# Optimization experiments

Hardware: AMD Instinct MI355X
Metric: run time of the kernel (lower is better)

The kernel has to match this reference:

```python
import jax, jax.numpy as jnp
import numpy as np

H = 128      # hidden_channels
G = 512      # number of graphs in the batch
NEG_SLOPE = 0.2


def _seg_sum(x, idx, n):
    return jax.ops.segment_sum(x, idx, num_segments=n)


def _sage(x_src, x_dst, ei, Wl, bl, Wr):
    # PyG SAGEConv: lin_l(mean_j x_j) + lin_r(x_i); lin_l has bias, lin_r does not.
    s, d = ei[0], ei[1]
    n = x_dst.shape[0]
    agg = _seg_sum(x_src[s], d, n)
    cnt = _seg_sum(jnp.ones((ei.shape[1],), x_src.dtype), d, n)
    mean = agg / jnp.maximum(cnt, 1.0)[:, None]
    return mean @ Wl + bl + x_dst @ Wr


def _gat(x_src, x_dst, ei, Ws, Wd, a_s, a_d, b):
    # PyG GATConv (heads=1, add_self_loops=False, bipartite): segment softmax over dst.
    s, d = ei[0], ei[1]
    n = x_dst.shape[0]
    hs = x_src @ Ws                                  # [N_src, H]
    hd = x_dst @ Wd                                  # [N_dst, H]
    logit = jax.nn.leaky_relu((hs @ a_s)[s] + (hd @ a_d)[d], NEG_SLOPE)
    m = jax.ops.segment_max(logit, d, num_segments=n)
    e = jnp.exp(logit - m[d])
    z = _seg_sum(e, d, n)
    alpha = e / jnp.maximum(z[d], 1e-16)
    return _seg_sum(alpha[:, None] * hs[s], d, n) + b


def _gcn(x, ei, W, b):
    # PyG GCNConv with add_self_loops=True, normalize=True (same src/dst node type).
    s, d = ei[0], ei[1]
    n = x.shape[0]
    deg = _seg_sum(jnp.ones((ei.shape[1],), x.dtype), d, n) + 1.0  # +1 self loop
    dis = jax.lax.rsqrt(deg)
    h = x @ W
    norm = dis[s] * dis[d]
    out = _seg_sum(norm[:, None] * h[s], d, n) + (dis * dis)[:, None] * h
    return out + b


def _pool(x, b):
    s = _seg_sum(x, b, G)
    c = _seg_sum(jnp.ones((x.shape[0],), x.dtype), b, G)
    return s / jnp.maximum(c, 1.0)[:, None]


def setup_inputs() -> dict:
    key = jax.random.key(0)
    ks = iter(jax.random.split(key, 80))
    scale = 1.0 / np.sqrt(H)

    def nrm(shape, sc=scale):
        return jax.random.normal(next(ks), shape, jnp.float32) * sc

    def edges(e, n_src, n_dst):
        src = jax.random.randint(next(ks), (e,), 0, n_src, jnp.int32)
        dst = jax.random.randint(next(ks), (e,), 0, n_dst, jnp.int32)
        return jnp.stack([src, dst])

    def batch(n):
        return jnp.sort(jax.random.randint(next(ks), (n,), 0, G, jnp.int32))

    N_CD, N_SEQ, N_ANNO, N_RANGE, N_MD = 100000, 80000, 80000, 80000, 50000
    inp = {
        'x_cd': nrm((N_CD, H), 1.0), 'x_seq': nrm((N_SEQ, H), 1.0),
        'x_anno': nrm((N_ANNO, H), 1.0), 'x_range': nrm((N_RANGE, H), 1.0),
        'x_md': nrm((N_MD, H), 1.0),
        'ei_seq': edges(160000, N_CD, N_SEQ),
        'ei_anno': edges(200000, N_CD, N_ANNO),
        'ei_range': edges(200000, N_CD, N_RANGE),
        'ei_comp': edges(300000, N_MD, N_CD),
        'ei_cc': edges(300000, N_CD, N_CD),
        'ei_mm': edges(150000, N_MD, N_MD),
        'b_cd': batch(N_CD), 'b_seq': batch(N_SEQ), 'b_anno': batch(N_ANNO),
        'b_range': batch(N_RANGE), 'b_md': batch(N_MD),
    }
    # per-layer stacked params (leading axis = 2 layers)
    for nm, shp in [('Wsl_seq', (2, H, H)), ('bs_seq', (2, H)), ('Wsr_seq', (2, H, H)),
                    ('Wsl_anno', (2, H, H)), ('bs_anno', (2, H)), ('Wsr_anno', (2, H, H)),
                    ('Wg_comp_s', (2, H, H)), ('Wg_comp_d', (2, H, H)),
                    ('ag_comp_s', (2, H)), ('ag_comp_d', (2, H)), ('bg_comp', (2, H)),
                    ('Wg_range_s', (2, H, H)), ('Wg_range_d', (2, H, H)),
                    ('ag_range_s', (2, H)), ('ag_range_d', (2, H)), ('bg_range', (2, H)),
                    ('Wc_cc', (2, H, H)), ('bc_cc', (2, H)),
                    ('Wc_mm', (2, H, H)), ('bc_mm', (2, H)),
                    ('lin1_W', (5 * H, H)), ('lin1_b', (H,)),
                    ('lin2_W', (H, 1)), ('lin2_b', (1,))]:
        inp[nm] = nrm(shp)
    return inp


def reference(x_cd, x_seq, x_anno, x_range, x_md,
              ei_seq, ei_anno, ei_range, ei_comp, ei_cc, ei_mm,
              b_cd, b_seq, b_anno, b_range, b_md,
              Wsl_seq, bs_seq, Wsr_seq, Wsl_anno, bs_anno, Wsr_anno,
              Wg_comp_s, Wg_comp_d, ag_comp_s, ag_comp_d, bg_comp,
              Wg_range_s, Wg_range_d, ag_range_s, ag_range_d, bg_range,
              Wc_cc, bc_cc, Wc_mm, bc_mm,
              lin1_W, lin1_b, lin2_W, lin2_b):
    for l in range(2):
        # HeteroConv aggr='sum': CD receives GAT(MD->CD) + GCN(CD->CD)
        n_cd = (_gat(x_md, x_cd, ei_comp, Wg_comp_s[l], Wg_comp_d[l],
                     ag_comp_s[l], ag_comp_d[l], bg_comp[l])
                + _gcn(x_cd, ei_cc, Wc_cc[l], bc_cc[l]))
        n_seq = _sage(x_cd, x_seq, ei_seq, Wsl_seq[l], bs_seq[l], Wsr_seq[l])
        n_anno = _sage(x_cd, x_anno, ei_anno, Wsl_anno[l], bs_anno[l], Wsr_anno[l])
        n_range = _gat(x_cd, x_range, ei_range, Wg_range_s[l], Wg_range_d[l],
                       ag_range_s[l], ag_range_d[l], bg_range[l])
        n_md = _gcn(x_md, ei_mm, Wc_mm[l], bc_mm[l])
        x_cd, x_seq, x_anno, x_range, x_md = (
            jax.nn.relu(n_cd), jax.nn.relu(n_seq), jax.nn.relu(n_anno),
            jax.nn.relu(n_range), jax.nn.relu(n_md))
    emb = jnp.concatenate([_pool(x_cd, b_cd), _pool(x_seq, b_seq),
                           _pool(x_anno, b_anno), _pool(x_range, b_range),
                           _pool(x_md, b_md)], axis=-1)        # [G, 5H]
    h = jax.nn.relu(emb @ lin1_W + lin1_b)  # Dropout(0.7) is identity in eval
    return (h @ lin2_W + lin2_b).reshape(-1)  # [G]
```

## Files before the change

kernel.cpp:

```cpp
#include <hip/hip_runtime.h>

#define HD 128
#define GNUM 512
#define RPB 520
#define IDXCAP 512
#define TM 32

typedef __attribute__((ext_vector_type(8))) short short8v;
typedef __attribute__((ext_vector_type(4))) float f32x4;

__device__ __forceinline__ void split1(float a, short& h, short& l) {
  unsigned u = __float_as_uint(a);
  unsigned hb = (u + 0x7FFFu + ((u >> 16) & 1u)) & 0xFFFF0000u;
  h = (short)(hb >> 16);
  float rest = a - __uint_as_float(hb);
  unsigned u2 = __float_as_uint(rest);
  l = (short)((u2 + 0x7FFFu + ((u2 >> 16) & 1u)) >> 16);
}

struct WTab { const float* p[8]; };
__global__ __launch_bounds__(256) void k_split_w(WTab tab, short* __restrict__ whi,
                                                 short* __restrict__ wlo)
{
  int m = blockIdx.x >> 6;
  int i = (blockIdx.x & 63) * 256 + threadIdx.x;
  const float* W = tab.p[m >> 1] + (m & 1) * 16384;
  int k = i >> 7, n = i & 127;
  short h, l;
  split1(W[k * 128 + n], h, l);
  whi[m * 16384 + n * 128 + k] = h;
  wlo[m * 16384 + n * 128 + k] = l;
}

#define CF_LD 132
__global__ __launch_bounds__(256) void k_gemm_conv(
    const float* __restrict__ A1, const short* __restrict__ WH1, const short* __restrict__ WL1,
    const int* __restrict__ grp, const int* __restrict__ gcol, int mode,
    const float* __restrict__ wsrc, const float* __restrict__ rowsc,
    const float* __restrict__ A2, const short* __restrict__ WH2, const short* __restrict__ WL2,
    float* __restrict__ C, const float* __restrict__ bias, const float* addin,
    int N, int relu,
    const float* __restrict__ avec, float* __restrict__ adot,
    const float* __restrict__ avec2, float* __restrict__ adot2)
{
  __shared__ char smem[TM * 136 * 2 * 2];
  __shared__ int idxbuf[IDXCAP];
  __shared__ float wbuf[IDXCAP];
  short* Ah = (short*)smem;
  short* Al = Ah + TM * 136;
  float* Cf = (float*)smem;

  const int t = threadIdx.x;
  const int row0 = blockIdx.x * TM;
  const int lane = t & 63, wid = t >> 6;
  const int g = lane >> 4, cn = lane & 15;
  const int colbase = wid * 32;

  f32x4 zero = {0.f, 0.f, 0.f, 0.f};
  f32x4 acc[2][2];
#pragma unroll
  for (int rt = 0; rt < 2; ++rt) { acc[rt][0] = zero; acc[rt][1] = zero; }

  auto storeAhl = [&](int row, int ln, float4 s) {
    short4 h, l;
    split1(s.x, h.x, l.x); split1(s.y, h.y, l.y);
    split1(s.z, h.z, l.z); split1(s.w, h.w, l.w);
    *(short4*)(Ah + row * 136 + ln * 4) = h;
    *(short4*)(Al + row * 136 + ln * 4) = l;
  };

  auto stageA = [&](const float* __restrict__ A) {
    const float4* A4 = (const float4*)(A + (size_t)row0 * 128);
#pragma unroll
    for (int i = 0; i < 4; ++i) {
      int f4 = t + i * 256;
      int row = f4 >> 5, c4 = f4 & 31;
      float4 v = make_float4(0.f, 0.f, 0.f, 0.f);
      if (row0 + row < N) v = A4[f4];
      storeAhl(row, c4, v);
    }
  };

  auto getcw = [&](int e, int e_lo, int& c, float& w) {
    int off = e - e_lo;
    if (off < IDXCAP) { c = idxbuf[off]; w = wbuf[off]; }
    else { c = gcol[e]; w = wsrc ? wsrc[c] : 0.f; }
  };

  auto stage_gather = [&](const float* __restrict__ X, int e_lo) {
#pragma unroll
    for (int i = 0; i < 4; ++i) {
      int f4 = t + i * 256;
      int row = f4 >> 5, ln = f4 & 31;
      int r = row0 + row;
      float4 s = make_float4(0.f, 0.f, 0.f, 0.f);
      int e0 = 0, e1 = 0;
      float rs = 0.f;
      if (r < N) {
        e0 = grp[r]; e1 = grp[r + 1];
        if (mode >= 2) rs = rowsc[r];
      }
      float z = 0.f;
      if (mode == 2 && r < N) {
        float4 xs_ = *(const float4*)(X + (size_t)r * 128 + ln * 4);
        float rr = rs * rs;
        s.x = rr * xs_.x; s.y = rr * xs_.y; s.z = rr * xs_.z; s.w = rr * xs_.w;
      }
      int e = e0;
      for (; e + 1 < e1; e += 2) {
        int c0, c1; float w0, w1;
        getcw(e, e_lo, c0, w0);
        getcw(e + 1, e_lo, c1, w1);
        float p0, p1;
        if (mode == 3) {
          float v0 = w0 + rs; v0 = v0 > 0.f ? v0 : 0.2f * v0;
          float v1 = w1 + rs; v1 = v1 > 0.f ? v1 : 0.2f * v1;
          p0 = __expf(v0); p1 = __expf(v1); z += p0 + p1;
        } else if (mode == 2) { p0 = w0 * rs; p1 = w1 * rs; }
        else { p0 = 1.f; p1 = 1.f; }
        float4 a = *(const float4*)(X + (size_t)c0 * 128 + ln * 4);
        float4 b = *(const float4*)(X + (size_t)c1 * 128 + ln * 4);
        s.x += p0 * a.x + p1 * b.x; s.y += p0 * a.y + p1 * b.y;
        s.z += p0 * a.z + p1 * b.z; s.w += p0 * a.w + p1 * b.w;
      }
      if (e < e1) {
        int c; float w;
        getcw(e, e_lo, c, w);
        float p;
        if (mode == 3) {
          float v = w + rs; v = v > 0.f ? v : 0.2f * v;
          p = __expf(v); z += p;
        } else if (mode == 2) p = w * rs;
        else p = 1.f;
        float4 a = *(const float4*)(X + (size_t)c * 128 + ln * 4);
        s.x += p * a.x; s.y += p * a.y; s.z += p * a.z; s.w += p * a.w;
      }
      if (mode == 1) {
        float inv = 1.f / fmaxf((float)(e1 - e0), 1.f);
        s.x *= inv; s.y *= inv; s.z *= inv; s.w *= inv;
      } else if (mode == 3) {
        float inv = (e1 > e0) ? 1.f / z : 0.f;
        s.x *= inv; s.y *= inv; s.z *= inv; s.w *= inv;
      }
      storeAhl(row, ln, s);
    }
  };

  auto accum = [&](const short* __restrict__ WH, const short* __restrict__ WL) {
#pragma unroll
    for (int kg = 0; kg < 4; ++kg) {
      short8v bhi[2], blo[2];
#pragma unroll
      for (int ct = 0; ct < 2; ++ct) {
        size_t o = (size_t)(colbase + ct * 16 + cn) * 128 + kg * 32 + g * 8;
        bhi[ct] = *(const short8v*)(WH + o);
        blo[ct] = *(const short8v*)(WL + o);
      }
#pragma unroll
      for (int rt = 0; rt < 2; ++rt) {
        const int ao = (rt * 16 + cn) * 136 + kg * 32 + g * 8;
        const short8v ah = *(const short8v*)(Ah + ao);
        const short8v al = *(const short8v*)(Al + ao);
#pragma unroll
        for (int ct = 0; ct < 2; ++ct) {
          acc[rt][ct] = __builtin_amdgcn_mfma_f32_16x16x32_bf16(ah, bhi[ct], acc[rt][ct], 0, 0, 0);
          acc[rt][ct] = __builtin_amdgcn_mfma_f32_16x16x32_bf16(al, bhi[ct], acc[rt][ct], 0, 0, 0);
          acc[rt][ct] = __builtin_amdgcn_mfma_f32_16x16x32_bf16(ah, blo[ct], acc[rt][ct], 0, 0, 0);
        }
      }
    }
  };

  if (mode != 0) {
    const int row_end = min(row0 + TM, N);
    const int e_lo = grp[row0];
    const int cnt = min(grp[row_end] - e_lo, IDXCAP);
    for (int k = t; k < cnt; k += 256) {
      int idx = gcol[e_lo + k];
      idxbuf[k] = idx;
      if (wsrc) wbuf[k] = wsrc[idx];
    }
    __syncthreads();
    stage_gather(A1, e_lo);
  } else {
    stageA(A1);
  }
  __syncthreads();
  accum(WH1, WL1);
  if (A2) {
    __syncthreads();
    stageA(A2);
    __syncthreads();
    accum(WH2, WL2);
  }
  __syncthreads();

#pragma unroll
  for (int rt = 0; rt < 2; ++rt)
#pragma unroll
    for (int ct = 0; ct < 2; ++ct)
#pragma unroll
      for (int r = 0; r < 4; ++r)
        Cf[(rt * 16 + g * 4 + r) * CF_LD + colbase + ct * 16 + cn] = acc[rt][ct][r];
  __syncthreads();

  float4* C4 = (float4*)(C + (size_t)row0 * 128);
#pragma unroll
  for (int i = 0; i < 4; ++i) {
    int f4 = t + i * 256;
    int row = f4 >> 5, c4 = f4 & 31;
    if (row0 + row < N) {
      float4 v = *(const float4*)(Cf + row * CF_LD + c4 * 4);
      if (bias) {
        float4 bv = *(const float4*)(bias + c4 * 4);
        v.x += bv.x; v.y += bv.y; v.z += bv.z; v.w += bv.w;
      }
      if (addin) {
        float4 av = *(const float4*)(addin + (size_t)(row0 + row) * 128 + c4 * 4);
        v.x += av.x; v.y += av.y; v.z += av.z; v.w += av.w;
      }
      if (relu) {
        v.x = fmaxf(v.x, 0.f); v.y = fmaxf(v.y, 0.f);
        v.z = fmaxf(v.z, 0.f); v.w = fmaxf(v.w, 0.f);
      }
      C4[f4] = v;
      if (avec) {
        float4 av = *(const float4*)(avec + c4 * 4);
        float p = v.x * av.x + v.y * av.y + v.z * av.z + v.w * av.w;
#pragma unroll
        for (int o = 1; o < 32; o <<= 1) p += __shfl_xor(p, o);
        if (c4 == 0) adot[row0 + row] = p;
      }
      if (avec2) {
        float4 av = *(const float4*)(avec2 + c4 * 4);
        float p = v.x * av.x + v.y * av.y + v.z * av.z + v.w * av.w;
#pragma unroll
        for (int o = 1; o < 32; o <<= 1) p += __shfl_xor(p, o);
        if (c4 == 0) adot2[row0 + row] = p;
      }
    }
  }
}

__global__ void k_rowdot(const float* __restrict__ x, const float* __restrict__ a,
                         float* __restrict__ out, int N)
{
  int wid = blockIdx.x * 4 + (threadIdx.x >> 6);
  int lane = threadIdx.x & 63;
  if (wid >= N) return;
  float2 xv = ((const float2*)x)[(size_t)wid * 64 + lane];
  float2 av = ((const float2*)a)[lane];
  float v = fmaf(xv.y, av.y, xv.x * av.x);
#pragma unroll
  for (int o = 32; o > 0; o >>= 1) v += __shfl_down(v, o);
  if (lane == 0) out[wid] = v;
}

__global__ void k_rowdot2(const float* __restrict__ x, const float* __restrict__ a1,
                          const float* __restrict__ a2, float* __restrict__ o1,
                          float* __restrict__ o2, int N)
{
  int wid = blockIdx.x * 4 + (threadIdx.x >> 6);
  int lane = threadIdx.x & 63;
  if (wid >= N) return;
  float2 xv = ((const float2*)x)[(size_t)wid * 64 + lane];
  float2 av1 = ((const float2*)a1)[lane];
  float2 av2 = ((const float2*)a2)[lane];
  float v1 = fmaf(xv.y, av1.y, xv.x * av1.x);
  float v2 = fmaf(xv.y, av2.y, xv.x * av2.x);
#pragma unroll
  for (int o = 32; o > 0; o >>= 1) { v1 += __shfl_down(v1, o); v2 += __shfl_down(v2, o); }
  if (lane == 0) { o1[wid] = v1; o2[wid] = v2; }
}

struct MTab { const float* W[8]; const float* a[8]; };
__global__ __launch_bounds__(128) void k_matvec8(MTab tb, float* __restrict__ wv)
{
  __shared__ float as[128];
  int m = blockIdx.x, i = threadIdx.x;
  as[i] = tb.a[m][i];
  __syncthreads();
  const float* W = tb.W[m];
  float v = 0.f;
  for (int j = 0; j < 128; ++j) v = fmaf(W[i * 128 + j], as[j], v);
  wv[m * 128 + i] = v;
}

struct HTab { const int* key[6]; int* cnt[6]; unsigned short* rank[6]; int bo[7]; int n[6]; };
__global__ void k_hist_rank_all(HTab tb) {
  int bi = blockIdx.x, ty = 0;
  while (ty < 5 && bi >= tb.bo[ty + 1]) ++ty;
  int i = (bi - tb.bo[ty]) * 256 + threadIdx.x;
  if (i < tb.n[ty])
    tb.rank[ty][i] = (unsigned short)atomicAdd(&tb.cnt[ty][tb.key[ty][i]], 1);
}

struct FTab { const int* es[6]; const int* ed[6]; const int* rp[6];
              const unsigned short* rank[6]; int* col[6]; int bo[7]; int n[6]; };
__global__ void k_fill_all(FTab tb) {
  int bi = blockIdx.x, ty = 0;
  while (ty < 5 && bi >= tb.bo[ty + 1]) ++ty;
  int e = (bi - tb.bo[ty]) * 256 + threadIdx.x;
  if (e >= tb.n[ty]) return;
  int p = tb.rp[ty][tb.ed[ty][e]] + (int)tb.rank[ty][e];
  tb.col[ty][p] = tb.es[ty][e];
}

struct STab { int* rp[6]; int* bs[6]; int n[6]; int bo[7]; };

__global__ __launch_bounds__(256) void k_scan_partial_all(STab tb) {
  __shared__ int red[256];
  int bi = blockIdx.x, ty = 0;
  while (ty < 5 && bi >= tb.bo[ty + 1]) ++ty;
  int lb = bi - tb.bo[ty];
  const int* rp = tb.rp[ty];
  const int N = tb.n[ty];
  const int t = threadIdx.x, base = lb * 4096;
  int s = 0;
  for (int i = t; i < 4096; i += 256) {
    int idx = base + i;
    if (idx < N) s += rp[idx];
  }
  red[t] = s;
  __syncthreads();
  for (int ofs = 128; ofs > 0; ofs >>= 1) {
    if (t < ofs) red[t] += red[t + ofs];
    __syncthreads();
  }
  if (t == 0) tb.bs[ty][lb] = red[0];
}

__global__ __launch_bounds__(256) void k_scan_bsums_all(STab tb) {
  __shared__ int sh[256];
  const int ty = blockIdx.x;
  const int nb = (tb.n[ty] + 4095) / 4096;
  const int t = threadIdx.x;
  int v = (t < nb) ? tb.bs[ty][t] : 0;
  sh[t] = v;
  __syncthreads();
  for (int ofs = 1; ofs < 256; ofs <<= 1) {
    int u = (t >= ofs) ? sh[t - ofs] : 0;
    __syncthreads();
    sh[t] += u;
    __syncthreads();
  }
  if (t < nb) tb.bs[ty][t] = sh[t] - v;
  if (t == 255) tb.rp[ty][tb.n[ty]] = sh[255];
}

__global__ __launch_bounds__(256) void k_scan_final_all(STab tb) {
  __shared__ int sh[4096 + 256];
  __shared__ int tsum[256];
  int bi = blockIdx.x, ty = 0;
  while (ty < 5 && bi >= tb.bo[ty + 1]) ++ty;
  int lb = bi - tb.bo[ty];
  int* rp = tb.rp[ty];
  const int N = tb.n[ty];
  const int t = threadIdx.x, base = lb * 4096;
  auto mp = [](int i) { return i + (i >> 4); };
#pragma unroll
  for (int i = 0; i < 16; ++i) {
    int idx = base + i * 256 + t;
    sh[mp(i * 256 + t)] = (idx < N) ? rp[idx] : 0;
  }
  __syncthreads();
  int s = 0;
#pragma unroll
  for (int j = 0; j < 16; ++j) s += sh[mp(t * 16 + j)];
  tsum[t] = s;
  __syncthreads();
  for (int ofs = 1; ofs < 256; ofs <<= 1) {
    int u = (t >= ofs) ? tsum[t - ofs] : 0;
    __syncthreads();
    tsum[t] += u;
    __syncthreads();
  }
  int pre = tsum[t] - s + tb.bs[ty][lb];
#pragma unroll
  for (int j = 0; j < 16; ++j) {
    int v = sh[mp(t * 16 + j)];
    sh[mp(t * 16 + j)] = pre;
    pre += v;
  }
  __syncthreads();
#pragma unroll
  for (int i = 0; i < 16; ++i) {
    int idx = base + i * 256 + t;
    if (idx < N) rp[idx] = sh[mp(i * 256 + t)];
  }
}

struct BTab { const int* b[5]; int n[5]; };
__global__ __launch_bounds__(512) void k_runptr(BTab tb, int* __restrict__ rpb_all) {
  const int ty = blockIdx.x;
  const int* b = tb.b[ty];
  const int N = tb.n[ty];
  const int t = threadIdx.x;
  int lo = 0, hi = N;
  while (lo < hi) {
    int mid = (lo + hi) >> 1;
    if (b[mid] < t) lo = mid + 1; else hi = mid;
  }
  rpb_all[ty * RPB + t] = lo;
  if (t == 0) rpb_all[ty * RPB + GNUM] = N;
}

struct DTab { const int* rp[2]; float* dis[2]; int n[2]; int bo[3]; };
__global__ void k_dis2(DTab tb) {
  int bi = blockIdx.x, ty = (bi >= tb.bo[1]) ? 1 : 0;
  int n = (bi - tb.bo[ty]) * 256 + threadIdx.x;
  if (n < tb.n[ty]) tb.dis[ty][n] = rsqrtf((float)(tb.rp[ty][n + 1] - tb.rp[ty][n]) + 1.f);
}

__global__ __launch_bounds__(256) void k_pool_seg(
    const float* __restrict__ x, const int* __restrict__ rpb,
    float* __restrict__ pool, int col_off)
{
  __shared__ float2 red2[4][64];
  const int g = blockIdx.x;
  const int t = threadIdx.x, w = t >> 6, lane = t & 63;
  const int n0 = rpb[g], n1 = rpb[g + 1];
  const float2* x2 = (const float2*)x;
  float a0 = 0.f, a1 = 0.f, b0 = 0.f, b1 = 0.f;
  int n = n0 + w;
  for (; n + 4 < n1; n += 8) {
    float2 vA = x2[(size_t)n * 64 + lane];
    float2 vB = x2[(size_t)(n + 4) * 64 + lane];
    a0 += vA.x; a1 += vA.y; b0 += vB.x; b1 += vB.y;
  }
  if (n < n1) { float2 vA = x2[(size_t)n * 64 + lane]; a0 += vA.x; a1 += vA.y; }
  red2[w][lane] = make_float2(a0 + b0, a1 + b1);
  __syncthreads();
  if (t < 64) {
    float2 r0 = red2[0][t], r1 = red2[1][t], r2 = red2[2][t], r3 = red2[3][t];
    float inv = 1.f / fmaxf((float)(n1 - n0), 1.f);
    ((float2*)(pool + (size_t)g * 640 + col_off))[t] =
        make_float2((r0.x + r1.x + r2.x + r3.x) * inv,
                    (r0.y + r1.y + r2.y + r3.y) * inv);
  }
}

__global__ void k_mlp(const float* __restrict__ pool,
                      const float* __restrict__ W1, const float* __restrict__ b1,
                      const float* __restrict__ W2, const float* __restrict__ b2,
                      float* __restrict__ out)
{
  __shared__ float emb[640];
  __shared__ float red[128];
  const int g = blockIdx.x, t = threadIdx.x;
  for (int i = t; i < 640; i += 128) emb[i] = pool[(size_t)g * 640 + i];
  __syncthreads();
  float acc = b1[t];
  for (int i = 0; i < 640; ++i) acc = fmaf(emb[i], W1[i * 128 + t], acc);
  float h = fmaxf(acc, 0.f);
  red[t] = h * W2[t];
  __syncthreads();
  for (int s = 64; s > 0; s >>= 1) {
    if (t < s) red[t] += red[t + s];
    __syncthreads();
  }
  if (t == 0) out[g] = red[0] + b2[0];
}

extern "C" void kernel_launch(void* const* d_in, const int* in_sizes, int n_in,
                              void* d_out, int out_size, void* d_ws, size_t ws_size,
                              hipStream_t stream)
{
  auto fin = [&](int i) { return (const float*)d_in[i]; };
  auto iin = [&](int i) { return (const int*)d_in[i]; };

  const float *x_cd = fin(0), *x_seq = fin(1), *x_anno = fin(2), *x_range = fin(3), *x_md = fin(4);
  const int *ei_seq = iin(5), *ei_anno = iin(6), *ei_range = iin(7),
            *ei_comp = iin(8), *ei_cc = iin(9), *ei_mm = iin(10);
  const int *b_cd = iin(11), *b_seq = iin(12), *b_anno = iin(13), *b_range = iin(14), *b_md = iin(15);

  const int N_CD = in_sizes[0] / HD, N_SEQ = in_sizes[1] / HD, N_ANNO = in_sizes[2] / HD,
            N_RANGE = in_sizes[3] / HD, N_MD = in_sizes[4] / HD;
  const int E_seq = in_sizes[5] / 2, E_anno = in_sizes[6] / 2, E_range = in_sizes[7] / 2,
            E_comp = in_sizes[8] / 2, E_cc = in_sizes[9] / 2, E_mm = in_sizes[10] / 2;
  const int N_OTH = max(max(N_SEQ, N_ANNO), N_RANGE);

  auto WLm = [&](int i, int l) { return fin(i) + (size_t)l * HD * HD; };
  auto WLv = [&](int i, int l) { return fin(i) + (size_t)l * HD; };

  float* ws = (float*)d_ws;
  size_t off = 0;
  auto alloc = [&](size_t n) { float* p = ws + off; off += (n + 3) & ~(size_t)3; return p; };
  float* xcd1 = alloc((size_t)N_CD * HD);
  float* xmd1 = alloc((size_t)N_MD * HD);
  float* xoth = alloc((size_t)N_OTH * HD);
  float* acc  = alloc((size_t)N_CD * HD);
  float* t1   = alloc((size_t)N_CD * HD);
  float* sA = alloc((size_t)N_CD);
  float* sB = alloc((size_t)N_CD);
  float* sC = alloc((size_t)N_CD);
  float* sD = alloc((size_t)N_CD);
  float* sE = alloc((size_t)N_CD);
  float* sF = alloc((size_t)N_CD);
  float* dis_cc = alloc((size_t)N_CD);
  float* dis_mm = alloc((size_t)N_MD);
  float* wv8 = alloc(8 * HD);
  float* pool = alloc((size_t)GNUM * 5 * HD);
  short* whi = (short*)(ws + off); off += (size_t)16 * 16384 / 2;
  short* wlo = (short*)(ws + off); off += (size_t)16 * 16384 / 2;
  auto alloci = [&](size_t n) { int* p = (int*)(ws + off); off += (n + 3) & ~(size_t)3; return p; };
  int* bsall = alloci(6 * 256);
  int* rpb_all = alloci(5 * RPB);
  int Nds[6] = {N_SEQ, N_ANNO, N_RANGE, N_CD, N_CD, N_MD};
  int Es[6]  = {E_seq, E_anno, E_range, E_comp, E_cc, E_mm};
  int* rps[6];
  int* rp0 = alloci(0);
  { size_t tot = 0; for (int i = 0; i < 6; ++i) tot += (size_t)Nds[i] + 1;
    int* p = alloci(tot); rp0 = p;
    for (int i = 0; i < 6; ++i) { rps[i] = p; p += Nds[i] + 1; } }
  size_t rp_tot_bytes = 0; for (int i = 0; i < 6; ++i) rp_tot_bytes += ((size_t)Nds[i] + 1) * 4;
  unsigned short* ranks[6];
  for (int i = 0; i < 6; ++i) ranks[i] = (unsigned short*)alloci(((size_t)Es[i] + 1) / 2);
  int* cols[6];  for (int i = 0; i < 6; ++i) cols[i] = alloci((size_t)Es[i]);
  (void)n_in;

  if (off * sizeof(float) > ws_size) {
    hipMemsetAsync(d_out, 0, (size_t)out_size * sizeof(float), stream);
    return;
  }

  auto ew = [&](size_t elems) { return dim3((unsigned)((elems + 255) / 256)); };
  auto nw = [&](int N) { return dim3((unsigned)((N + 3) / 4)); };

  WTab tab;
  tab.p[0] = fin(16); tab.p[1] = fin(18); tab.p[2] = fin(19); tab.p[3] = fin(21);
  tab.p[4] = fin(22); tab.p[5] = fin(27); tab.p[6] = fin(32); tab.p[7] = fin(34);
  k_split_w<<<dim3(1024), dim3(256), 0, stream>>>(tab, whi, wlo);

  MTab mt;
  mt.W[0] = WLm(22, 0); mt.a[0] = WLv(24, 0);
  mt.W[1] = WLm(23, 0); mt.a[1] = WLv(25, 0);
  mt.W[2] = WLm(22, 1); mt.a[2] = WLv(24, 1);
  mt.W[3] = WLm(23, 1); mt.a[3] = WLv(25, 1);
  mt.W[4] = WLm(27, 0); mt.a[4] = WLv(29, 0);
  mt.W[5] = WLm(28, 0); mt.a[5] = WLv(30, 0);
  mt.W[6] = WLm(27, 1); mt.a[6] = WLv(29, 1);
  mt.W[7] = WLm(28, 1); mt.a[7] = WLv(30, 1);
  k_matvec8<<<dim3(8), dim3(128), 0, stream>>>(mt, wv8);

  k_rowdot<<<nw(N_MD), dim3(256), 0, stream>>>(x_md, wv8 + 0 * 128, sA, N_MD);
  k_rowdot2<<<nw(N_CD), dim3(256), 0, stream>>>(x_cd, wv8 + 1 * 128, wv8 + 4 * 128,
                                                sB, sC, N_CD);
  k_rowdot<<<nw(N_RANGE), dim3(256), 0, stream>>>(x_range, wv8 + 5 * 128, sD, N_RANGE);

  {
    BTab bt;
    bt.b[0] = b_cd; bt.n[0] = N_CD;  bt.b[1] = b_seq; bt.n[1] = N_SEQ;
    bt.b[2] = b_anno; bt.n[2] = N_ANNO;  bt.b[3] = b_range; bt.n[3] = N_RANGE;
    bt.b[4] = b_md; bt.n[4] = N_MD;
    k_runptr<<<dim3(5), dim3(512), 0, stream>>>(bt, rpb_all);
  }

  const int* ess[6] = {ei_seq, ei_anno, ei_range, ei_comp, ei_cc, ei_mm};
  const int* eds[6] = {ei_seq + E_seq, ei_anno + E_anno, ei_range + E_range,
                       ei_comp + E_comp, ei_cc + E_cc, ei_mm + E_mm};
  hipMemsetAsync(rp0, 0, rp_tot_bytes, stream);
  {
    HTab ht; int b = 0;
    for (int i = 0; i < 6; ++i) {
      ht.key[i] = eds[i]; ht.cnt[i] = rps[i]; ht.rank[i] = ranks[i];
      ht.bo[i] = b; b += (Es[i] + 255) / 256; ht.n[i] = Es[i];
    }
    ht.bo[6] = b;
    k_hist_rank_all<<<dim3(b), dim3(256), 0, stream>>>(ht);
  }
  {
    STab st; int b = 0;
    for (int i = 0; i < 6; ++i) {
      st.rp[i] = rps[i]; st.bs[i] = bsall + i * 256;
      st.n[i] = Nds[i]; st.bo[i] = b; b += (Nds[i] + 4095) / 4096;
    }
    st.bo[6] = b;
    k_scan_partial_all<<<dim3(b), dim3(256), 0, stream>>>(st);
    k_scan_bsums_all<<<dim3(6), dim3(256), 0, stream>>>(st);
    k_scan_final_all<<<dim3(b), dim3(256), 0, stream>>>(st);
  }
  {
    FTab ft; int b = 0;
    for (int i = 0; i < 6; ++i) {
      ft.es[i] = ess[i]; ft.ed[i] = eds[i]; ft.rp[i] = rps[i]; ft.rank[i] = ranks[i];
      ft.col[i] = cols[i]; ft.bo[i] = b; b += (Es[i] + 255) / 256; ft.n[i] = Es[i];
    }
    ft.bo[6] = b;
    k_fill_all<<<dim3(b), dim3(256), 0, stream>>>(ft);
  }
  int *rp_seq = rps[0], *rp_anno = rps[1], *rp_range = rps[2],
      *rp_comp = rps[3], *rp_cc = rps[4], *rp_mm = rps[5];
  int *col_seq = cols[0], *col_anno = cols[1], *col_range = cols[2],
      *col_comp = cols[3], *col_cc = cols[4], *col_mm = cols[5];
  {
    DTab dt;
    dt.rp[0] = rp_cc; dt.dis[0] = dis_cc; dt.n[0] = N_CD;
    dt.rp[1] = rp_mm; dt.dis[1] = dis_mm; dt.n[1] = N_MD;
    dt.bo[0] = 0; dt.bo[1] = (N_CD + 255) / 256;
    dt.bo[2] = dt.bo[1] + (N_MD + 255) / 256;
    k_dis2<<<dim3(dt.bo[2]), dim3(256), 0, stream>>>(dt);
  }

  auto WHp = [&](int sidx, int layer) { return whi + (size_t)(sidx * 2 + layer) * 16384; };
  auto WLp = [&](int sidx, int layer) { return wlo + (size_t)(sidx * 2 + layer) * 16384; };

  auto conv = [&](int mode, const float* A1, int sidx, int layer,
                  const int* grp, const int* gcol,
                  const float* wsrc, const float* rowsc,
                  const float* A2, int sidx2,
                  float* C, const float* bias, const float* addin, int N, int relu,
                  const float* avec, float* adot, const float* avec2, float* adot2) {
    k_gemm_conv<<<dim3((N + TM - 1) / TM), dim3(256), 0, stream>>>(
        A1, WHp(sidx, layer), WLp(sidx, layer), grp, gcol, mode, wsrc, rowsc,
        A2, A2 ? WHp(sidx2, layer) : nullptr, A2 ? WLp(sidx2, layer) : nullptr,
        C, bias, addin, N, relu, avec, adot, avec2, adot2);
  };
  auto do_pool = [&](const float* x, int type) {
    k_pool_seg<<<dim3(GNUM), dim3(256), 0, stream>>>(x, rpb_all + type * RPB, pool, type * HD);
  };

  conv(3, x_md, 4, 0, rp_comp, col_comp, sA, sB, nullptr, 0,
       acc, WLv(26, 0), nullptr, N_CD, 0, nullptr, nullptr, nullptr, nullptr);
  conv(2, x_cd, 6, 0, rp_cc, col_cc, dis_cc, dis_cc, nullptr, 0,
       xcd1, WLv(33, 0), acc, N_CD, 1, wv8 + 3 * 128, sB, wv8 + 6 * 128, sE);
  conv(2, x_md, 7, 0, rp_mm, col_mm, dis_mm, dis_mm, nullptr, 0,
       xmd1, WLv(35, 0), nullptr, N_MD, 1, wv8 + 2 * 128, sA, nullptr, nullptr);
  conv(3, xmd1, 4, 1, rp_comp, col_comp, sA, sB, nullptr, 0,
       acc, WLv(26, 1), nullptr, N_CD, 0, nullptr, nullptr, nullptr, nullptr);
  conv(2, xcd1, 6, 1, rp_cc, col_cc, dis_cc, dis_cc, nullptr, 0,
       acc, WLv(33, 1), acc, N_CD, 1, nullptr, nullptr, nullptr, nullptr);
  do_pool(acc, 0);
  conv(2, xmd1, 7, 1, rp_mm, col_mm, dis_mm, dis_mm, nullptr, 0,
       acc, WLv(35, 1), nullptr, N_MD, 1, nullptr, nullptr, nullptr, nullptr);
  do_pool(acc, 4);

  conv(1, x_cd, 0, 0, rp_seq, col_seq, nullptr, nullptr, x_seq, 1,
       xoth, WLv(17, 0), nullptr, N_SEQ, 1, nullptr, nullptr, nullptr, nullptr);
  conv(1, xcd1, 0, 1, rp_seq, col_seq, nullptr, nullptr, xoth, 1,
       acc, WLv(17, 1), nullptr, N_SEQ, 1, nullptr, nullptr, nullptr, nullptr);
  do_pool(acc, 1);
  conv(1, x_cd, 2, 0, rp_anno, col_anno, nullptr, nullptr, x_anno, 3,
       t1, WLv(20, 0), nullptr, N_ANNO, 1, nullptr, nullptr, nullptr, nullptr);
  conv(1, xcd1, 2, 1, rp_anno, col_anno, nullptr, nullptr, t1, 3,
       acc, WLv(20, 1), nullptr, N_ANNO, 1, nullptr, nullptr, nullptr, nullptr);
  do_pool(acc, 2);
  conv(3, x_cd, 5, 0, rp_range, col_range, sC, sD, nullptr, 0,
       xoth, WLv(31, 0), nullptr, N_RANGE, 1, wv8 + 7 * 128, sF, nullptr, nullptr);
  conv(3, xcd1, 5, 1, rp_range, col_range, sE, sF, nullptr, 0,
       acc, WLv(31, 1), nullptr, N_RANGE, 1, nullptr, nullptr, nullptr, nullptr);
  do_pool(acc, 3);

  k_mlp<<<dim3(GNUM), dim3(128), 0, stream>>>(
      pool, fin(36), fin(37), fin(38), fin(39), (float*)d_out);
}
```

Baseline: 923.7 us.

## Fuse GAT and GCN convolutions for CD nodes into one kernel launch

Generalizes the conv kernel to take two operand descriptors, each with its own gather mode, so the GAT(MD->CD) and GCN(CD->CD) passes that feed the CD nodes run in one launch and sum in registers. This removes the intermediate accumulator write and read plus a kernel launch per layer. It also prefetches the second operand's edge indices into shared memory while the first MFMA accumulation runs. The cost is a larger kernel body, a second bias, and possible register pressure.

```diff
diff --git a/kernel.cpp b/kernel.cpp
--- a/kernel.cpp
+++ b/kernel.cpp
@@ -32,14 +32,16 @@
   wlo[m * 16384 + n * 128 + k] = l;
 }
 
+struct COp {
+  const float* A; const short* WH; const short* WL;
+  const int* grp; const int* gcol;
+  const float* wsrc; const float* rowsc; int mode;
+};
 #define CF_LD 132
 __global__ __launch_bounds__(256) void k_gemm_conv(
-    const float* __restrict__ A1, const short* __restrict__ WH1, const short* __restrict__ WL1,
-    const int* __restrict__ grp, const int* __restrict__ gcol, int mode,
-    const float* __restrict__ wsrc, const float* __restrict__ rowsc,
-    const float* __restrict__ A2, const short* __restrict__ WH2, const short* __restrict__ WL2,
-    float* __restrict__ C, const float* __restrict__ bias, const float* addin,
-    int N, int relu,
+    COp o0, COp o1, int hasO1,
+    float* __restrict__ C, const float* __restrict__ bias, const float* __restrict__ bias2,
+    const float* addin, int N, int relu,
     const float* __restrict__ avec, float* __restrict__ adot,
     const float* __restrict__ avec2, float* __restrict__ adot2)
 {
@@ -70,24 +72,36 @@
   };
 
   auto stageA = [&](const float* __restrict__ A) {
-    const float4* A4 = (const float4*)(A + (size_t)row0 * 128);
 #pragma unroll
     for (int i = 0; i < 4; ++i) {
       int f4 = t + i * 256;
       int row = f4 >> 5, c4 = f4 & 31;
       float4 v = make_float4(0.f, 0.f, 0.f, 0.f);
-      if (row0 + row < N) v = A4[f4];
+      if (row0 + row < N) v = ((const float4*)(A + (size_t)row0 * 128))[f4];
       storeAhl(row, c4, v);
     }
   };
 
-  auto getcw = [&](int e, int e_lo, int& c, float& w) {
-    int off = e - e_lo;
-    if (off < IDXCAP) { c = idxbuf[off]; w = wbuf[off]; }
-    else { c = gcol[e]; w = wsrc ? wsrc[c] : 0.f; }
-  };
-
-  auto stage_gather = [&](const float* __restrict__ X, int e_lo) {
+  auto prefetch = [&](const COp& op) {
+    const int row_end = min(row0 + TM, N);
+    const int e_lo = op.grp[row0];
+    const int cnt = min(op.grp[row_end] - e_lo, IDXCAP);
+    for (int k = t; k < cnt; k += 256) {
+      int idx = op.gcol[e_lo + k];
+      idxbuf[k] = idx;
+      if (op.wsrc) wbuf[k] = op.wsrc[idx];
+    }
+  };
+
+  auto stage_gather = [&](const COp& op) {
+    const int e_lo = op.grp[row0];
+    const int mode = op.mode;
+    const float* X = op.A;
+    auto getcw = [&](int e, int& c, float& w) {
+      int off = e - e_lo;
+      if (off < IDXCAP) { c = idxbuf[off]; w = wbuf[off]; }
+      else { c = op.gcol[e]; w = op.wsrc ? op.wsrc[c] : 0.f; }
+    };
 #pragma unroll
     for (int i = 0; i < 4; ++i) {
       int f4 = t + i * 256;
@@ -97,8 +111,8 @@
       int e0 = 0, e1 = 0;
       float rs = 0.f;
       if (r < N) {
-        e0 = grp[r]; e1 = grp[r + 1];
-        if (mode >= 2) rs = rowsc[r];
+        e0 = op.grp[r]; e1 = op.grp[r + 1];
+        if (mode >= 2) rs = op.rowsc[r];
       }
       float z = 0.f;
       if (mode == 2 && r < N) {
@@ -109,8 +123,8 @@
       int e = e0;
       for (; e + 1 < e1; e += 2) {
         int c0, c1; float w0, w1;
-        getcw(e, e_lo, c0, w0);
-        getcw(e + 1, e_lo, c1, w1);
+        getcw(e, c0, w0);
+        getcw(e + 1, c1, w1);
         float p0, p1;
         if (mode == 3) {
           float v0 = w0 + rs; v0 = v0 > 0.f ? v0 : 0.2f * v0;
@@ -125,7 +139,7 @@
       }
       if (e < e1) {
         int c; float w;
-        getcw(e, e_lo, c, w);
+        getcw(e, c, w);
         float p;
         if (mode == 3) {
           float v = w + rs; v = v > 0.f ? v : 0.2f * v;
@@ -171,27 +185,21 @@
     }
   };
 
-  if (mode != 0) {
-    const int row_end = min(row0 + TM, N);
-    const int e_lo = grp[row0];
-    const int cnt = min(grp[row_end] - e_lo, IDXCAP);
-    for (int k = t; k < cnt; k += 256) {
-      int idx = gcol[e_lo + k];
-      idxbuf[k] = idx;
-      if (wsrc) wbuf[k] = wsrc[idx];
-    }
-    __syncthreads();
-    stage_gather(A1, e_lo);
+  if (o0.mode) {
+    prefetch(o0);
+    __syncthreads();
+    stage_gather(o0);
   } else {
-    stageA(A1);
-  }
-  __syncthreads();
-  accum(WH1, WL1);
-  if (A2) {
-    __syncthreads();
-    stageA(A2);
-    __syncthreads();
-    accum(WH2, WL2);
+    stageA(o0.A);
+  }
+  __syncthreads();
+  if (hasO1 && o1.mode) prefetch(o1);
+  accum(o0.WH, o0.WL);
+  if (hasO1) {
+    __syncthreads();
+    if (o1.mode) stage_gather(o1); else stageA(o1.A);
+    __syncthreads();
+    accum(o1.WH, o1.WL);
   }
   __syncthreads();
 
@@ -213,6 +221,10 @@
       float4 v = *(const float4*)(Cf + row * CF_LD + c4 * 4);
       if (bias) {
         float4 bv = *(const float4*)(bias + c4 * 4);
+        v.x += bv.x; v.y += bv.y; v.z += bv.z; v.w += bv.w;
+      }
+      if (bias2) {
+        float4 bv = *(const float4*)(bias2 + c4 * 4);
         v.x += bv.x; v.y += bv.y; v.z += bv.z; v.w += bv.w;
       }
       if (addin) {
@@ -605,50 +617,62 @@
   auto WHp = [&](int sidx, int layer) { return whi + (size_t)(sidx * 2 + layer) * 16384; };
   auto WLp = [&](int sidx, int layer) { return wlo + (size_t)(sidx * 2 + layer) * 16384; };
 
-  auto conv = [&](int mode, const float* A1, int sidx, int layer,
+  auto mkop = [&](int mode, const float* A, int sidx, int layer,
                   const int* grp, const int* gcol,
-                  const float* wsrc, const float* rowsc,
-                  const float* A2, int sidx2,
-                  float* C, const float* bias, const float* addin, int N, int relu,
-                  const float* avec, float* adot, const float* avec2, float* adot2) {
+                  const float* wsrc, const float* rowsc) {
+    COp o;
+    o.A = A; o.WH = WHp(sidx, layer); o.WL = WLp(sidx, layer);
+    o.grp = grp; o.gcol = gcol; o.wsrc = wsrc; o.rowsc = rowsc; o.mode = mode;
+    return o;
+  };
+  auto launch = [&](COp o0, COp o1, int hasO1, float* C, const float* bias,
+                    const float* bias2, const float* addin, int N, int relu,
+                    const float* avec, float* adot, const float* avec2, float* adot2) {
     k_gemm_conv<<<dim3((N + TM - 1) / TM), dim3(256), 0, stream>>>(
-        A1, WHp(sidx, layer), WLp(sidx, layer), grp, gcol, mode, wsrc, rowsc,
-        A2, A2 ? WHp(sidx2, layer) : nullptr, A2 ? WLp(sidx2, layer) : nullptr,
-        C, bias, addin, N, relu, avec, adot, avec2, adot2);
+        o0, o1, hasO1, C, bias, bias2, addin, N, relu, avec, adot, avec2, adot2);
   };
   auto do_pool = [&](const float* x, int type) {
     k_pool_seg<<<dim3(GNUM), dim3(256), 0, stream>>>(x, rpb_all + type * RPB, pool, type * HD);
   };
-
-  conv(3, x_md, 4, 0, rp_comp, col_comp, sA, sB, nullptr, 0,
-       acc, WLv(26, 0), nullptr, N_CD, 0, nullptr, nullptr, nullptr, nullptr);
-  conv(2, x_cd, 6, 0, rp_cc, col_cc, dis_cc, dis_cc, nullptr, 0,
-       xcd1, WLv(33, 0), acc, N_CD, 1, wv8 + 3 * 128, sB, wv8 + 6 * 128, sE);
-  conv(2, x_md, 7, 0, rp_mm, col_mm, dis_mm, dis_mm, nullptr, 0,
-       xmd1, WLv(35, 0), nullptr, N_MD, 1, wv8 + 2 * 128, sA, nullptr, nullptr);
-  conv(3, xmd1, 4, 1, rp_comp, col_comp, sA, sB, nullptr, 0,
-       acc, WLv(26, 1), nullptr, N_CD, 0, nullptr, nullptr, nullptr, nullptr);
-  conv(2, xcd1, 6, 1, rp_cc, col_cc, dis_cc, dis_cc, nullptr, 0,
-       acc, WLv(33, 1), acc, N_CD, 1, nullptr, nullptr, nullptr, nullptr);
+  COp nop = {};
+
+  launch(mkop(3, x_md, 4, 0, rp_comp, col_comp, sA, sB),
+         mkop(2, x_cd, 6, 0, rp_cc, col_cc, dis_cc, dis_cc), 1,
+         xcd1, WLv(26, 0), WLv(33, 0), nullptr, N_CD, 1,
+         wv8 + 3 * 128, sB, wv8 + 6 * 128, sE);
+  launch(mkop(2, x_md, 7, 0, rp_mm, col_mm, dis_mm, dis_mm), nop, 0,
+         xmd1, WLv(35, 0), nullptr, nullptr, N_MD, 1,
+         wv8 + 2 * 128, sA, nullptr, nullptr);
+  launch(mkop(3, xmd1, 4, 1, rp_comp, col_comp, sA, sB),
+         mkop(2, xcd1, 6, 1, rp_cc, col_cc, dis_cc, dis_cc), 1,
+         acc, WLv(26, 1), WLv(33, 1), nullptr, N_CD, 1,
+         nullptr, nullptr, nullptr, nullptr);
   do_pool(acc, 0);
-  conv(2, xmd1, 7, 1, rp_mm, col_mm, dis_mm, dis_mm, nullptr, 0,
-       acc, WLv(35, 1), nullptr, N_MD, 1, nullptr, nullptr, nullptr, nullptr);
+  launch(mkop(2, xmd1, 7, 1, rp_mm, col_mm, dis_mm, dis_mm), nop, 0,
+         acc, WLv(35, 1), nullptr, nullptr, N_MD, 1,
+         nullptr, nullptr, nullptr, nullptr);
   do_pool(acc, 4);
 
-  conv(1, x_cd, 0, 0, rp_seq, col_seq, nullptr, nullptr, x_seq, 1,
-       xoth, WLv(17, 0), nullptr, N_SEQ, 1, nullptr, nullptr, nullptr, nullptr);
-  conv(1, xcd1, 0, 1, rp_seq, col_seq, nullptr, nullptr, xoth, 1,
-       acc, WLv(17, 1), nullptr, N_SEQ, 1, nullptr, nullptr, nullptr, nullptr);
+  launch(mkop(1, x_cd, 0, 0, rp_seq, col_seq, nullptr, nullptr),
+         mkop(0, x_seq, 1, 0, nullptr, nullptr, nullptr, nullptr), 1,
+         xoth, WLv(17, 0), nullptr, nullptr, N_SEQ, 1, nullptr, nullptr, nullptr, nullptr);
+  launch(mkop(1, xcd1, 0, 1, rp_seq, col_seq, nullptr, nullptr),
+         mkop(0, xoth, 1, 1, nullptr, nullptr, nullptr, nullptr), 1,
+         acc, WLv(17, 1), nullptr, nullptr, N_SEQ, 1, nullptr, nullptr, nullptr, nullptr);
   do_pool(acc, 1);
-  conv(1, x_cd, 2, 0, rp_anno, col_anno, nullptr, nullptr, x_anno, 3,
-       t1, WLv(20, 0), nullptr, N_ANNO, 1, nullptr, nullptr, nullptr, nullptr);
-  conv(1, xcd1, 2, 1, rp_anno, col_anno, nullptr, nullptr, t1, 3,
-       acc, WLv(20, 1), nullptr, N_ANNO, 1, nullptr, nullptr, nullptr, nullptr);
+  launch(mkop(1, x_cd, 2, 0, rp_anno, col_anno, nullptr, nullptr),
+         mkop(0, x_anno, 3, 0, nullptr, nullptr, nullptr, nullptr), 1,
+         t1, WLv(20, 0), nullptr, nullptr, N_ANNO, 1, nullptr, nullptr, nullptr, nullptr);
+  launch(mkop(1, xcd1, 2, 1, rp_anno, col_anno, nullptr, nullptr),
+         mkop(0, t1, 3, 1, nullptr, nullptr, nullptr, nullptr), 1,
+         acc, WLv(20, 1), nullptr, nullptr, N_ANNO, 1, nullptr, nullptr, nullptr, nullptr);
   do_pool(acc, 2);
-  conv(3, x_cd, 5, 0, rp_range, col_range, sC, sD, nullptr, 0,
-       xoth, WLv(31, 0), nullptr, N_RANGE, 1, wv8 + 7 * 128, sF, nullptr, nullptr);
-  conv(3, xcd1, 5, 1, rp_range, col_range, sE, sF, nullptr, 0,
-       acc, WLv(31, 1), nullptr, N_RANGE, 1, nullptr, nullptr, nullptr, nullptr);
+  launch(mkop(3, x_cd, 5, 0, rp_range, col_range, sC, sD), nop, 0,
+         xoth, WLv(31, 0), nullptr, nullptr, N_RANGE, 1,
+         wv8 + 7 * 128, sF, nullptr, nullptr);
+  launch(mkop(3, xcd1, 5, 1, rp_range, col_range, sE, sF), nop, 0,
+         acc, WLv(31, 1), nullptr, nullptr, N_RANGE, 1,
+         nullptr, nullptr, nullptr, nullptr);
   do_pool(acc, 3);
 
   k_mlp<<<dim3(GNUM), dim3(128), 0, stream>>>(
```

After: 884.4 us. -4.3%, faster.
